# Kernel optimization log

Measured on AMD Instinct MI355X. Metric: run time of the kernel, lower is better.

Reference implementation:

```python
import jax, jax.numpy as jnp
import numpy as np

NB_TS = 4          # module-level global nb_timestep in the original code
EMBED = 512
SQRT_DIM = float(np.sqrt(EMBED))


def _conv(x, w, b=None):
    # torch Conv2d(kernel=3, stride=1, padding=1), NCHW / OIHW
    y = jax.lax.conv_general_dilated(x, w, (1, 1), ((1, 1), (1, 1)),
                                     dimension_numbers=('NCHW', 'OIHW', 'NCHW'))
    if b is not None:
        y = y + b[None, :, None, None]
    return y


def setup_inputs() -> dict:
    B, C, H, W = 8, 512, 16, 16
    TXT = 256
    key = jax.random.key(0)
    ks = iter(jax.random.split(key, 40))

    def nrm(shape, s=0.02):
        return jax.random.normal(next(ks), shape, jnp.float32) * s

    inp = {
        'x':   jax.random.normal(next(ks), (B, C, H, W), jnp.float32),
        'txt': jax.random.normal(next(ks), (B, 1, TXT), jnp.float32),
        # attention convs
        'Wa_w': nrm((C, C, 3, 3)), 'Wa_b': nrm((C,)),
        'Ua_w': nrm((C, C, 3, 3)), 'Ua_b': nrm((C,)),
        'Va_w': nrm((1, C, 3, 3)),
        # gate convs
        'Wi_w': nrm((C, C, 3, 3)), 'Wi_b': nrm((C,)),
        'Ui_w': nrm((C, C, 3, 3)), 'Ui_b': nrm((C,)),
        'Wf_w': nrm((C, C, 3, 3)), 'Wf_b': nrm((C,)),
        'Uf_w': nrm((C, C, 3, 3)), 'Uf_b': nrm((C,)),
        'Wc_w': nrm((C, C, 3, 3)), 'Wc_b': nrm((C,)),
        'Uc_w': nrm((C, C, 3, 3)), 'Uc_b': nrm((C,)),
        'Wo_w': nrm((C, C, 3, 3)), 'Wo_b': nrm((C,)),
        'Uo_w': nrm((C, C, 3, 3)), 'Uo_b': nrm((C,)),
        # text attention linears (torch Linear weight layout [out, in])
        'WQ': nrm((EMBED * H * W, TXT)),
        'WK': nrm((EMBED, 1)),
        'WV': nrm((EMBED, 1)),
        'Wsum_w': nrm((1, EMBED)), 'Wsum_b': nrm((1,)),
    }
    return inp


def reference(x, txt, Wa_w, Wa_b, Ua_w, Ua_b, Va_w,
              Wi_w, Wi_b, Ui_w, Ui_b, Wf_w, Wf_b, Uf_w, Uf_b,
              Wc_w, Wc_b, Uc_w, Uc_b, Wo_w, Wo_b, Uo_w, Uo_b,
              WQ, WK, WV, Wsum_w, Wsum_b):
    B, _, Hs, Ws = x.shape
    txt2 = txt.reshape(txt.shape[0], txt.shape[2])  # [B, 256]
    h = x
    c = x
    # Q is timestep-invariant; hoist out of the loop (same math)
    Q = (txt2 @ WQ.T).reshape(B, Hs, Ws, EMBED)  # [B,H,W,E]
    for _ in range(NB_TS):
        Z = _conv(jnp.tanh(_conv(h, Wa_w, Wa_b) + _conv(x, Ua_w, Ua_b)), Va_w)  # [B,1,H,W]
        A1 = jax.nn.softmax(Z, axis=1)          # softmax over channel dim of size 1 (faithful)
        Ap = jnp.transpose(A1, (0, 2, 3, 1))    # [B,H,W,1]
        K = Ap @ WK.T                            # [B,H,W,E]
        V = Ap @ WV.T                            # [B,H,W,E]
        scores = jnp.sum(Q * K, axis=3, keepdims=True) / SQRT_DIM  # [B,H,W,1]
        attn = jax.nn.softmax(scores, axis=1)    # torch softmax(dim=1) -> over H axis
        # repeat(...,embed_dim)*V is just a broadcast multiply
        A2 = (attn * V) @ Wsum_w.T + Wsum_b      # [B,H,W,1]
        A2 = jnp.transpose(A2, (0, 3, 1, 2))     # [B,1,H,W]
        myA = A1 + A2
        AM = myA * x
        i = jax.nn.sigmoid(_conv(AM, Wi_w, Wi_b) + _conv(h, Ui_w, Ui_b))
        f = jax.nn.sigmoid(_conv(AM, Wf_w, Wf_b) + _conv(h, Uf_w, Uf_b))
        o = jax.nn.sigmoid(_conv(AM, Wo_w, Wo_b) + _conv(h, Uo_w, Uo_b))
        g = jnp.tanh(_conv(AM, Wc_w, Wc_b) + _conv(h, Uc_w, Uc_b))
        c = g * i + f * c
        h = jnp.tanh(c) * o
    return h
```

## Files before the change

### kernel.cpp

```cpp
#include <hip/hip_runtime.h>

typedef unsigned short u16;
typedef __attribute__((ext_vector_type(8))) _Float16 f16x8;
typedef __attribute__((ext_vector_type(4))) float f32x4;
typedef __attribute__((ext_vector_type(4))) int i32x4;
typedef __attribute__((ext_vector_type(4))) unsigned short us4;

__device__ __forceinline__ u16 f2h(float f) {
  _Float16 h = (_Float16)f;
  return __builtin_bit_cast(unsigned short, h);
}
__device__ __forceinline__ float sigm(float v) { return 1.0f / (1.0f + __expf(-v)); }
__device__ __forceinline__ float tanh_(float v) {
  float t = __expf(-2.0f * fabsf(v));
  float r = (1.0f - t) / (1.0f + t);
  return v >= 0.0f ? r : -r;
}

typedef const __attribute__((address_space(1))) unsigned int* gas_t;
typedef __attribute__((address_space(3))) unsigned int* las_t;
__device__ __forceinline__ void gl16(const u16* g, u16* l) {
  __builtin_amdgcn_global_load_lds((gas_t)g, (las_t)l, 16, 0, 0);
}

__global__ __launch_bounds__(256, 2) void prep_big(
    const float* __restrict__ WQ, const float* __restrict__ WK,
    const float* __restrict__ txt, const float* __restrict__ WV,
    const float* __restrict__ Wsw, const float* __restrict__ Wsb,
    const float* __restrict__ wi, const float* __restrict__ wf,
    const float* __restrict__ wo, const float* __restrict__ wc,
    const float* __restrict__ ui, const float* __restrict__ uf,
    const float* __restrict__ uo, const float* __restrict__ uc,
    u16* __restrict__ dstW, u16* __restrict__ dstU,
    float* __restrict__ scores, float* __restrict__ sb) {
  __shared__ float red[4][8];
  __shared__ float red2[4];
  int tid = threadIdx.x;
  if (blockIdx.x < 2048) {
    int p = blockIdx.x & 255;
    int es = blockIdx.x >> 8;
    int t4 = tid & 63, eg = tid >> 6;
    f32x4 wkq[4];
    const f32x4* wkp = (const f32x4*)(WK + es * 64 + eg * 16);
#pragma unroll
    for (int i = 0; i < 4; ++i) wkq[i] = wkp[i];
    const f32x4* base = (const f32x4*)WQ + (size_t)(p * 512 + es * 64 + eg * 16) * 64 + t4;
    f32x4 m4 = {0.f, 0.f, 0.f, 0.f};
#pragma unroll
    for (int i = 0; i < 4; ++i) {
#pragma unroll
      for (int e = 0; e < 4; ++e) {
        f32x4 qv = base[(i * 4 + e) * 64];
        m4 += qv * wkq[i][e];
      }
    }
    float v[8];
    const f32x4* txp = (const f32x4*)txt;
#pragma unroll
    for (int b = 0; b < 8; ++b) {
      f32x4 tx = txp[b * 64 + t4];
      v[b] = m4[0] * tx[0] + m4[1] * tx[1] + m4[2] * tx[2] + m4[3] * tx[3];
    }
#pragma unroll
    for (int off = 32; off; off >>= 1)
#pragma unroll
      for (int b = 0; b < 8; ++b) v[b] += __shfl_down(v[b], off, 64);
    if (t4 == 0)
#pragma unroll
      for (int b = 0; b < 8; ++b) red[eg][b] = v[b];
    __syncthreads();
    if (tid < 8) {
      float sv = red[0][tid] + red[1][tid] + red[2][tid] + red[3][tid];
      atomicAdd(&scores[tid * 256 + p], sv * 0.044194173824159216f);
    }
    if (blockIdx.x == 0) {
      float vv = WV[tid] * Wsw[tid] + WV[tid + 256] * Wsw[tid + 256];
#pragma unroll
      for (int off = 32; off; off >>= 1) vv += __shfl_down(vv, off, 64);
      if (t4 == 0) red2[eg] = vv;
      __syncthreads();
      if (tid == 0) {
        sb[0] = red2[0] + red2[1] + red2[2] + red2[3];
        sb[1] = Wsb[0];
      }
    }
    return;
  }
  int sbid = blockIdx.x - 2048;
  int set = sbid >> 9;
  int chgrp = (sbid >> 4) & 31;
  int chunk = sbid & 15;
  int q = tid & 3, gch = tid >> 2;
  int gate = gch >> 4, chrow = gch & 15;
  int ch = chgrp * 16 + chrow;
  const float* s;
  if (set == 0) s = gate == 0 ? wi : gate == 1 ? wf : gate == 2 ? wo : wc;
  else          s = gate == 0 ? ui : gate == 1 ? uf : gate == 2 ? uo : uc;
  const f32x4* src = (const f32x4*)(s + (size_t)(ch * 512 + chunk * 32) * 9) + q * 18;
  f32x4 va[18];
#pragma unroll
  for (int i = 0; i < 18; ++i) va[i] = src[i];
  u16* dst = (set == 0 ? dstW : dstU) + (size_t)(chgrp * 16 + chunk) * 18432
             + (size_t)(gate * 64 + q * 16 + chrow) * 8;
#pragma unroll
  for (int k9 = 0; k9 < 9; ++k9) {
    i32x4 wv;
#pragma unroll
    for (int w = 0; w < 4; ++w) {
      int i0 = (2 * w) * 9 + k9, i1 = (2 * w + 1) * 9 + k9;
      unsigned lo = f2h(va[i0 >> 2][i0 & 3]);
      unsigned hi = f2h(va[i1 >> 2][i1 & 3]);
      wv[w] = (int)(lo | (hi << 16));
    }
    *(i32x4*)(dst + k9 * 2048) = wv;
  }
}

__global__ void prep_inputs(const float* __restrict__ x, const float* __restrict__ scores,
                            const float* __restrict__ sb,
                            u16* __restrict__ AM, u16* __restrict__ H0) {
  __shared__ float sc[16];
  int idx = blockIdx.x * 256 + threadIdx.x;
  int ch = idx & 511, p = (idx >> 9) & 255, b = idx >> 17;
  int w = p & 15, h = p >> 4;
  if (threadIdx.x < 16) sc[threadIdx.x] = scores[b * 256 + threadIdx.x * 16 + w];
  __syncthreads();
  float s = sb[0], b0 = sb[1];
  float mx = -1e30f;
#pragma unroll
  for (int hh = 0; hh < 16; ++hh) mx = fmaxf(mx, sc[hh]);
  float den = 0.f, my = 0.f;
#pragma unroll
  for (int hh = 0; hh < 16; ++hh) {
    float e = __expf(sc[hh] - mx);
    den += e;
    if (hh == h) my = e;
  }
  float coef = 1.0f + b0 + s * my / den;
  float xv = x[(size_t)(b * 512 + ch) * 256 + p];
  AM[idx] = f2h(coef * xv);
  H0[idx] = f2h(xv);
}

template <int MODE>
__launch_bounds__(256, 2)
__global__ void conv4(const u16* __restrict__ inA, const u16* __restrict__ inH,
                      const u16* __restrict__ wW, const u16* __restrict__ wU,
                      const float* __restrict__ bWi, const float* __restrict__ bUi,
                      const float* __restrict__ bWf, const float* __restrict__ bUf,
                      const float* __restrict__ bWo, const float* __restrict__ bUo,
                      const float* __restrict__ bWc, const float* __restrict__ bUc,
                      float* __restrict__ G, const float* __restrict__ c_src,
                      float* __restrict__ c_dst, u16* __restrict__ h_out,
                      float* __restrict__ out) {
  __shared__ __align__(16) u16 Alds[9 * 4 * 64 * 8];
  __shared__ __align__(16) u16 Blds[10 * 18 * 32];
  const int tid = threadIdx.x;
  const int chgrp = blockIdx.x & 31;
  const int nhalf = (blockIdx.x >> 5) & 1;
  const int b = blockIdx.x >> 6;
  const int wave = tid >> 6, lane = tid & 63;
  const int row = lane & 15, quad = lane >> 4;
  const int NCH = (MODE == 0) ? 32 : 16;
  const int gyBase = nhalf * 8 - 1;

  {
    i32x4 z = {0, 0, 0, 0};
    i32x4* bz = (i32x4*)Blds;
#pragma unroll
    for (int i = 0; i < 3; ++i) {
      int k = tid + 256 * i;
      if (k < 720) bz[k] = z;
    }
  }
  __syncthreads();

  const u16* wsrcW = wW + (size_t)chgrp * 294912;
  const u16* wsrcU = wU + (size_t)chgrp * 294912;
  const u16* isrcA = inA + (size_t)b * 131072;
  const u16* isrcH = inH + (size_t)b * 131072;

  auto stage = [&](int k) {
    const u16* gw;
    const u16* gi;
    if (MODE == 0 && k < 16) { gw = wsrcW + k * 18432; gi = isrcA + k * 32; }
    else                     { gw = wsrcU + (k & 15) * 18432; gi = isrcH + (k & 15) * 32; }
#pragma unroll
    for (int i = 0; i < 9; ++i)
      gl16(gw + (i * 256 + tid) * 8, &Alds[(i * 256 + wave * 64) * 8]);
    int xi = lane >> 2;
    int qsrc = (lane & 3) ^ (((xi + 1) >> 2) & 3);
#pragma unroll
    for (int j = 0; j < 3; ++j) {
      int r = j * 4 + wave;
      int gy = gyBase + r;
      if (r < 10 && gy >= 0 && gy < 16)
        gl16(gi + (size_t)(gy * 16 + xi) * 512 + qsrc * 8,
             &Blds[r * 576 + 32]);
    }
  };

  f32x4 acc[4][2];
#pragma unroll
  for (int m = 0; m < 4; ++m)
#pragma unroll
    for (int n = 0; n < 2; ++n) acc[m][n] = (f32x4){0.f, 0.f, 0.f, 0.f};

  const int ch0 = chgrp * 16 + quad * 4;
  float* gptr = G + (size_t)blockIdx.x * 8192 + wave * 2048 + lane * 4;

  stage(0);
  __syncthreads();

#pragma unroll 1
  for (int k = 0; k < NCH; ++k) {
#pragma unroll
    for (int kx = 0; kx < 3; ++kx) {
      int xx = row + kx;
      int qs = quad ^ ((xx >> 2) & 3);
      f16x8 bfr[4];
#pragma unroll
      for (int jj = 0; jj < 4; ++jj)
        bfr[jj] = *(const f16x8*)(&Blds[(wave * 2 + jj) * 576 + xx * 32 + qs * 8]);
#pragma unroll
      for (int ky = 0; ky < 3; ++ky) {
#pragma unroll
        for (int m = 0; m < 4; ++m) {
          f16x8 af = *(const f16x8*)(&Alds[((ky * 3 + kx) * 4 + m) * 512 + lane * 8]);
#pragma unroll
          for (int n = 0; n < 2; ++n)
            acc[m][n] = __builtin_amdgcn_mfma_f32_16x16x32_f16(af, bfr[n + ky], acc[m][n], 0, 0, 0);
        }
      }
    }
    if constexpr (MODE == 0) {
      if (k == 15) {
#pragma unroll
        for (int m = 0; m < 4; ++m) {
          const float* bw = m == 0 ? bWi : m == 1 ? bWf : m == 2 ? bWo : bWc;
          const float* bu = m == 0 ? bUi : m == 1 ? bUf : m == 2 ? bUo : bUc;
          f32x4 bias;
#pragma unroll
          for (int r = 0; r < 4; ++r) bias[r] = bw[ch0 + r] + bu[ch0 + r];
#pragma unroll
          for (int n = 0; n < 2; ++n) {
            acc[m][n] = acc[m][n] + bias;
            *(f32x4*)(gptr + (m * 2 + n) * 256) = acc[m][n];
          }
        }
      }
    }
    if (k + 1 < NCH) {
      __syncthreads();
      stage(k + 1);
      __syncthreads();
    }
  }

#pragma unroll
  for (int n = 0; n < 2; ++n) {
    const int p = (nhalf * 8 + wave * 2 + n) * 16 + row;
    f32x4 zi = acc[0][n], zf = acc[1][n], zo = acc[2][n], zg = acc[3][n];
    if constexpr (MODE != 0) {
      zi = zi + *(const f32x4*)(gptr + (0 + n) * 256);
      zf = zf + *(const f32x4*)(gptr + (2 + n) * 256);
      zo = zo + *(const f32x4*)(gptr + (4 + n) * 256);
      zg = zg + *(const f32x4*)(gptr + (6 + n) * 256);
    }
    f32x4 cold;
#pragma unroll
    for (int r = 0; r < 4; ++r)
      cold[r] = c_src[(size_t)(b * 512 + ch0 + r) * 256 + p];
    f32x4 cnew, hv;
#pragma unroll
    for (int r = 0; r < 4; ++r) {
      float iv = sigm(zi[r]);
      float fv = sigm(zf[r]);
      float ov = sigm(zo[r]);
      float gv = tanh_(zg[r]);
      float cn = fmaf(gv, iv, fv * cold[r]);
      cnew[r] = cn;
      hv[r] = tanh_(cn) * ov;
    }
    if constexpr (MODE != 2) {
#pragma unroll
      for (int r = 0; r < 4; ++r)
        c_dst[(size_t)(b * 512 + ch0 + r) * 256 + p] = cnew[r];
      us4 hb;
      hb[0] = f2h(hv[0]); hb[1] = f2h(hv[1]);
      hb[2] = f2h(hv[2]); hb[3] = f2h(hv[3]);
      *(us4*)(h_out + (size_t)b * 131072 + (size_t)p * 512 + ch0) = hb;
    } else {
#pragma unroll
      for (int r = 0; r < 4; ++r)
        out[(size_t)(b * 512 + ch0 + r) * 256 + p] = hv[r];
    }
  }
}

extern "C" void kernel_launch(void* const* d_in, const int* in_sizes, int n_in,
                              void* d_out, int out_size, void* d_ws, size_t ws_size,
                              hipStream_t stream) {
  const float* x    = (const float*)d_in[0];
  const float* txt  = (const float*)d_in[1];
  const float* Wi_w = (const float*)d_in[7];
  const float* Wi_b = (const float*)d_in[8];
  const float* Ui_w = (const float*)d_in[9];
  const float* Ui_b = (const float*)d_in[10];
  const float* Wf_w = (const float*)d_in[11];
  const float* Wf_b = (const float*)d_in[12];
  const float* Uf_w = (const float*)d_in[13];
  const float* Uf_b = (const float*)d_in[14];
  const float* Wc_w = (const float*)d_in[15];
  const float* Wc_b = (const float*)d_in[16];
  const float* Uc_w = (const float*)d_in[17];
  const float* Uc_b = (const float*)d_in[18];
  const float* Wo_w = (const float*)d_in[19];
  const float* Wo_b = (const float*)d_in[20];
  const float* Uo_w = (const float*)d_in[21];
  const float* Uo_b = (const float*)d_in[22];
  const float* WQ   = (const float*)d_in[23];
  const float* WK   = (const float*)d_in[24];
  const float* WV   = (const float*)d_in[25];
  const float* Wsw  = (const float*)d_in[26];
  const float* Wsb  = (const float*)d_in[27];
  (void)in_sizes; (void)n_in; (void)ws_size;

  char* ws = (char*)d_ws;
  size_t off = 0;
  auto carve = [&](size_t n) {
    char* p = ws + off;
    off += (n + 255) & ~(size_t)255;
    return p;
  };
  u16* WswzW    = (u16*)carve(18874368);
  u16* WswzU    = (u16*)carve(18874368);
  u16* AM       = (u16*)carve(2097152);
  u16* H0       = (u16*)carve(2097152);
  u16* H1       = (u16*)carve(2097152);
  float* G      = (float*)carve(16777216);
  float* C      = (float*)carve(4194304);
  float* scores = (float*)carve(8192);
  float* sb     = (float*)carve(256);

  hipMemsetAsync(scores, 0, 8192, stream);

  prep_big<<<3072, 256, 0, stream>>>(WQ, WK, txt, WV, Wsw, Wsb,
                                     Wi_w, Wf_w, Wo_w, Wc_w,
                                     Ui_w, Uf_w, Uo_w, Uc_w,
                                     WswzW, WswzU, scores, sb);
  prep_inputs<<<4096, 256, 0, stream>>>(x, scores, sb, AM, H0);

  conv4<0><<<512, 256, 0, stream>>>(AM, H0, WswzW, WswzU,
                                    Wi_b, Ui_b, Wf_b, Uf_b, Wo_b, Uo_b, Wc_b, Uc_b,
                                    G, x, C, H1, nullptr);
  conv4<1><<<512, 256, 0, stream>>>(nullptr, H1, nullptr, WswzU,
                                    nullptr, nullptr, nullptr, nullptr,
                                    nullptr, nullptr, nullptr, nullptr,
                                    G, C, C, H0, nullptr);
  conv4<1><<<512, 256, 0, stream>>>(nullptr, H0, nullptr, WswzU,
                                    nullptr, nullptr, nullptr, nullptr,
                                    nullptr, nullptr, nullptr, nullptr,
                                    G, C, C, H1, nullptr);
  conv4<2><<<512, 256, 0, stream>>>(nullptr, H1, nullptr, WswzU,
                                    nullptr, nullptr, nullptr, nullptr,
                                    nullptr, nullptr, nullptr, nullptr,
                                    G, C, nullptr, nullptr, (float*)d_out);
}
```

Measured before the change: 502.9 us.

## Double-buffer conv LDS staging and merge spatial halves into 512-thread blocks

The gate conv kernel now double-buffers weight and input tiles in LDS, issuing the next channel chunk's async loads before computing the current one, so there is one barrier per iteration instead of two. Each block now covers the full 16x16 image with 8 waves instead of two half-image blocks, which halves weight re-staging per output. This halves the grid to 256 blocks and doubles LDS use per block, which may reduce occupancy and the number of CUs kept busy. The prep kernel also hoists all WQ loads ahead of the FMAs and raises its occupancy hint.

```diff
diff --git a/kernel.cpp b/kernel.cpp
--- a/kernel.cpp
+++ b/kernel.cpp
@@ -23,7 +23,7 @@
   __builtin_amdgcn_global_load_lds((gas_t)g, (las_t)l, 16, 0, 0);
 }
 
-__global__ __launch_bounds__(256, 2) void prep_big(
+__global__ __launch_bounds__(256, 4) void prep_big(
     const float* __restrict__ WQ, const float* __restrict__ WK,
     const float* __restrict__ txt, const float* __restrict__ WV,
     const float* __restrict__ Wsw, const float* __restrict__ Wsb,
@@ -40,20 +40,19 @@
     int p = blockIdx.x & 255;
     int es = blockIdx.x >> 8;
     int t4 = tid & 63, eg = tid >> 6;
+    const f32x4* base = (const f32x4*)WQ + ((size_t)p * 512 + es * 64 + eg * 16) * 64 + t4;
+    f32x4 va[16];
+#pragma unroll
+    for (int i = 0; i < 16; ++i) va[i] = base[i * 64];
     f32x4 wkq[4];
     const f32x4* wkp = (const f32x4*)(WK + es * 64 + eg * 16);
 #pragma unroll
     for (int i = 0; i < 4; ++i) wkq[i] = wkp[i];
-    const f32x4* base = (const f32x4*)WQ + (size_t)(p * 512 + es * 64 + eg * 16) * 64 + t4;
     f32x4 m4 = {0.f, 0.f, 0.f, 0.f};
 #pragma unroll
-    for (int i = 0; i < 4; ++i) {
-#pragma unroll
-      for (int e = 0; e < 4; ++e) {
-        f32x4 qv = base[(i * 4 + e) * 64];
-        m4 += qv * wkq[i][e];
-      }
-    }
+    for (int i = 0; i < 4; ++i)
+#pragma unroll
+      for (int e = 0; e < 4; ++e) m4 += va[i * 4 + e] * wkq[i][e];
     float v[8];
     const f32x4* txp = (const f32x4*)txt;
 #pragma unroll
@@ -143,7 +142,7 @@
 }
 
 template <int MODE>
-__launch_bounds__(256, 2)
+__launch_bounds__(512, 2)
 __global__ void conv4(const u16* __restrict__ inA, const u16* __restrict__ inH,
                       const u16* __restrict__ wW, const u16* __restrict__ wU,
                       const float* __restrict__ bWi, const float* __restrict__ bUi,
@@ -153,24 +152,22 @@
                       float* __restrict__ G, const float* __restrict__ c_src,
                       float* __restrict__ c_dst, u16* __restrict__ h_out,
                       float* __restrict__ out) {
-  __shared__ __align__(16) u16 Alds[9 * 4 * 64 * 8];
-  __shared__ __align__(16) u16 Blds[10 * 18 * 32];
+  __shared__ __align__(16) u16 Alds[2][9 * 4 * 64 * 8];
+  __shared__ __align__(16) u16 Blds[2][18 * 18 * 32];
   const int tid = threadIdx.x;
   const int chgrp = blockIdx.x & 31;
-  const int nhalf = (blockIdx.x >> 5) & 1;
-  const int b = blockIdx.x >> 6;
+  const int b = blockIdx.x >> 5;
   const int wave = tid >> 6, lane = tid & 63;
   const int row = lane & 15, quad = lane >> 4;
   const int NCH = (MODE == 0) ? 32 : 16;
-  const int gyBase = nhalf * 8 - 1;
 
   {
     i32x4 z = {0, 0, 0, 0};
-    i32x4* bz = (i32x4*)Blds;
-#pragma unroll
-    for (int i = 0; i < 3; ++i) {
-      int k = tid + 256 * i;
-      if (k < 720) bz[k] = z;
+    i32x4* bz = (i32x4*)&Blds[0][0];
+#pragma unroll
+    for (int i = 0; i < 6; ++i) {
+      int k = tid + 512 * i;
+      if (k < 2592) bz[k] = z;
     }
   }
   __syncthreads();
@@ -180,23 +177,24 @@
   const u16* isrcA = inA + (size_t)b * 131072;
   const u16* isrcH = inH + (size_t)b * 131072;
 
-  auto stage = [&](int k) {
+  auto stage = [&](int k, int bb) {
     const u16* gw;
     const u16* gi;
     if (MODE == 0 && k < 16) { gw = wsrcW + k * 18432; gi = isrcA + k * 32; }
     else                     { gw = wsrcU + (k & 15) * 18432; gi = isrcH + (k & 15) * 32; }
-#pragma unroll
-    for (int i = 0; i < 9; ++i)
-      gl16(gw + (i * 256 + tid) * 8, &Alds[(i * 256 + wave * 64) * 8]);
+    u16* Ab = &Alds[bb][0];
+#pragma unroll
+    for (int i = 0; i < 5; ++i) {
+      int idx = i * 8 + wave;
+      if (idx < 36) gl16(gw + (idx * 64 + lane) * 8, &Ab[idx * 512]);
+    }
+    u16* Bb = &Blds[bb][0];
     int xi = lane >> 2;
     int qsrc = (lane & 3) ^ (((xi + 1) >> 2) & 3);
 #pragma unroll
-    for (int j = 0; j < 3; ++j) {
-      int r = j * 4 + wave;
-      int gy = gyBase + r;
-      if (r < 10 && gy >= 0 && gy < 16)
-        gl16(gi + (size_t)(gy * 16 + xi) * 512 + qsrc * 8,
-             &Blds[r * 576 + 32]);
+    for (int j = 0; j < 2; ++j) {
+      int gy = wave + j * 8;
+      gl16(gi + (size_t)(gy * 16 + xi) * 512 + qsrc * 8, &Bb[(gy + 1) * 576 + 32]);
     }
   };
 
@@ -207,13 +205,17 @@
     for (int n = 0; n < 2; ++n) acc[m][n] = (f32x4){0.f, 0.f, 0.f, 0.f};
 
   const int ch0 = chgrp * 16 + quad * 4;
-  float* gptr = G + (size_t)blockIdx.x * 8192 + wave * 2048 + lane * 4;
-
-  stage(0);
+  float* gptr = G + (size_t)blockIdx.x * 16384 + wave * 2048 + lane * 4;
+
+  stage(0, 0);
   __syncthreads();
+  int bb = 0;
 
 #pragma unroll 1
   for (int k = 0; k < NCH; ++k) {
+    if (k + 1 < NCH) stage(k + 1, bb ^ 1);
+    const u16* Ab = &Alds[bb][0];
+    const u16* Bb = &Blds[bb][0];
 #pragma unroll
     for (int kx = 0; kx < 3; ++kx) {
       int xx = row + kx;
@@ -221,12 +223,12 @@
       f16x8 bfr[4];
 #pragma unroll
       for (int jj = 0; jj < 4; ++jj)
-        bfr[jj] = *(const f16x8*)(&Blds[(wave * 2 + jj) * 576 + xx * 32 + qs * 8]);
+        bfr[jj] = *(const f16x8*)(&Bb[(wave * 2 + jj) * 576 + xx * 32 + qs * 8]);
 #pragma unroll
       for (int ky = 0; ky < 3; ++ky) {
 #pragma unroll
         for (int m = 0; m < 4; ++m) {
-          f16x8 af = *(const f16x8*)(&Alds[((ky * 3 + kx) * 4 + m) * 512 + lane * 8]);
+          f16x8 af = *(const f16x8*)(&Ab[((ky * 3 + kx) * 4 + m) * 512 + lane * 8]);
 #pragma unroll
           for (int n = 0; n < 2; ++n)
             acc[m][n] = __builtin_amdgcn_mfma_f32_16x16x32_f16(af, bfr[n + ky], acc[m][n], 0, 0, 0);
@@ -250,16 +252,13 @@
         }
       }
     }
-    if (k + 1 < NCH) {
-      __syncthreads();
-      stage(k + 1);
-      __syncthreads();
-    }
+    __syncthreads();
+    bb ^= 1;
   }
 
 #pragma unroll
   for (int n = 0; n < 2; ++n) {
-    const int p = (nhalf * 8 + wave * 2 + n) * 16 + row;
+    const int p = (wave * 2 + n) * 16 + row;
     f32x4 zi = acc[0][n], zf = acc[1][n], zo = acc[2][n], zg = acc[3][n];
     if constexpr (MODE != 0) {
       zi = zi + *(const f32x4*)(gptr + (0 + n) * 256);
@@ -351,18 +350,18 @@
                                      WswzW, WswzU, scores, sb);
   prep_inputs<<<4096, 256, 0, stream>>>(x, scores, sb, AM, H0);
 
-  conv4<0><<<512, 256, 0, stream>>>(AM, H0, WswzW, WswzU,
+  conv4<0><<<256, 512, 0, stream>>>(AM, H0, WswzW, WswzU,
                                     Wi_b, Ui_b, Wf_b, Uf_b, Wo_b, Uo_b, Wc_b, Uc_b,
                                     G, x, C, H1, nullptr);
-  conv4<1><<<512, 256, 0, stream>>>(nullptr, H1, nullptr, WswzU,
+  conv4<1><<<256, 512, 0, stream>>>(nullptr, H1, nullptr, WswzU,
                                     nullptr, nullptr, nullptr, nullptr,
                                     nullptr, nullptr, nullptr, nullptr,
                                     G, C, C, H0, nullptr);
-  conv4<1><<<512, 256, 0, stream>>>(nullptr, H0, nullptr, WswzU,
+  conv4<1><<<256, 512, 0, stream>>>(nullptr, H0, nullptr, WswzU,
                                     nullptr, nullptr, nullptr, nullptr,
                                     nullptr, nullptr, nullptr, nullptr,
                                     G, C, C, H1, nullptr);
-  conv4<2><<<512, 256, 0, stream>>>(nullptr, H1, nullptr, WswzU,
+  conv4<2><<<256, 512, 0, stream>>>(nullptr, H1, nullptr, WswzU,
                                     nullptr, nullptr, nullptr, nullptr,
                                     nullptr, nullptr, nullptr, nullptr,
                                     G, C, nullptr, nullptr, (float*)d_out);
```

After: 516.2 us. 1.03x slower.
